# Kernel optimization log

Measured on AMD Instinct MI355X. Metric: run time of the kernel, lower is better.

The kernel has to match this reference:

```python
import jax, jax.numpy as jnp
import numpy as np

N_NODES = 50000
IN_F, HID_F, OUT_F = 256, 128, 40
N_EDGES = 800000


def _uniform(key, shape, scale):
    return jax.random.uniform(key, shape, dtype=jnp.float32, minval=-scale, maxval=scale)


def setup_inputs() -> dict:
    key = jax.random.key(0)
    ks = jax.random.split(key, 20)
    x = jax.random.normal(ks[0], (N_NODES, IN_F), dtype=jnp.float32)
    edge_index = jax.random.randint(ks[1], (2, N_EDGES), 0, N_NODES, dtype=jnp.int64)
    s0, sa0 = 1.0 / np.sqrt(HID_F), 1.0  # std_att = 1/sqrt(1)
    s1, sa1 = 1.0 / np.sqrt(OUT_F), 1.0
    sv = 1.0 / np.sqrt(3.0)
    return {
        "x": x, "edge_index": edge_index,
        "Wl0": _uniform(ks[2], (IN_F, HID_F), s0),
        "Wh0": _uniform(ks[3], (IN_F, HID_F), s0),
        "Wm0": _uniform(ks[4], (IN_F, HID_F), s0),
        "al0": _uniform(ks[5], (HID_F, 1), sa0),
        "ah0": _uniform(ks[6], (HID_F, 1), sa0),
        "am0": _uniform(ks[7], (HID_F, 1), sa0),
        "att0": _uniform(ks[8], (3, 3), sv),
        "Wl1": _uniform(ks[9], (HID_F, OUT_F), s1),
        "Wh1": _uniform(ks[10], (HID_F, OUT_F), s1),
        "Wm1": _uniform(ks[11], (HID_F, OUT_F), s1),
        "al1": _uniform(ks[12], (OUT_F, 1), sa1),
        "ah1": _uniform(ks[13], (OUT_F, 1), sa1),
        "am1": _uniform(ks[14], (OUT_F, 1), sa1),
        "att1": _uniform(ks[15], (3, 3), sv),
    }


def _acm_layer(x, row, col, d_inv, Wl, Wh, Wm, al, ah, am, att):
    n = x.shape[0]
    hl, hh, hm = x @ Wl, x @ Wh, x @ Wm
    # adj_low @ M  with adj_low = D^{-1}(I + A): gather sources, scatter-add to rows
    def low(M):
        return d_inv[:, None] * (M + jax.ops.segment_sum(M[col], row, num_segments=n))
    out_low = jax.nn.relu(low(hl))
    out_high = jax.nn.relu(hh - low(hh))  # adj_high = I - adj_low
    out_mlp = jax.nn.relu(hm)
    T = 3.0
    sig = jax.nn.sigmoid(jnp.concatenate([out_low @ al, out_high @ ah, out_mlp @ am], axis=1))  # [n,3]
    a = jax.nn.softmax((sig @ att) / T, axis=1)
    return 3.0 * (a[:, 0:1] * out_low + a[:, 1:2] * out_high + a[:, 2:3] * out_mlp)


def reference(x, edge_index, Wl0, Wh0, Wm0, al0, ah0, am0, att0,
              Wl1, Wh1, Wm1, al1, ah1, am1, att1):
    n = x.shape[0]
    row, col = edge_index[0], edge_index[1]
    deg = jax.ops.segment_sum(jnp.ones_like(row, dtype=jnp.float32), row, num_segments=n)
    rowsum = 1.0 + deg  # rowsum of I + A (duplicates counted, as in scipy)
    d_inv = jnp.where(rowsum > 0, 1.0 / rowsum, 0.0)
    h = _acm_layer(x, row, col, d_inv, Wl0, Wh0, Wm0, al0, ah0, am0, att0)
    out = _acm_layer(h, row, col, d_inv, Wl1, Wh1, Wm1, al1, ah1, am1, att1)
    return out
```

## Files before the change

kernel.cpp:

```cpp
#include <hip/hip_runtime.h>
#include <math.h>

#define N_NODES 50000
#define N_EDGES 800000
#define IN_F    256
#define HID_F   128
#define OUT_F   40
#define W0N     (3*HID_F)
#define W1N     (3*OUT_F)
#define NB      ((N_NODES + 255) / 256)

#define XB   6250
#define P0B  ((IN_F * W0N) / 256)
#define P1B  ((HID_F * W1N) / 256)
#define CB0  (XB + P0B + P1B)
#define CNTB ((N_EDGES + 255) / 256)
#define PREPB (CB0 + CNTB)

typedef __attribute__((ext_vector_type(8))) unsigned short ushort8;
typedef __attribute__((ext_vector_type(4))) unsigned short ushort4v;
typedef __attribute__((ext_vector_type(8))) __bf16 bf16x8;
typedef __attribute__((ext_vector_type(4))) float f32x4;
typedef __attribute__((ext_vector_type(2))) float f32x2;

static __device__ __forceinline__ float sigmoidf_(float x) {
    return 1.0f / (1.0f + expf(-x));
}

static __device__ __forceinline__ unsigned short f2bf(float f) {
    unsigned u = __float_as_uint(f);
    u += 0x7FFFu + ((u >> 16) & 1u);
    return (unsigned short)(u >> 16);
}

static __device__ __forceinline__ float bflo(unsigned u) { return __uint_as_float(u << 16); }
static __device__ __forceinline__ float bfhi(unsigned u) { return __uint_as_float(u & 0xffff0000u); }


__global__ __launch_bounds__(256) void k_prep(
        const float* __restrict__ x, unsigned short* __restrict__ xb,
        const float* __restrict__ Wl0, const float* __restrict__ Wh0,
        const float* __restrict__ Wm0, unsigned short* __restrict__ W0t,
        const float* __restrict__ Wl1, const float* __restrict__ Wh1,
        const float* __restrict__ Wm1, unsigned short* __restrict__ W1t,
        const int* __restrict__ ei, int* __restrict__ deg,
        unsigned short* __restrict__ rank, unsigned* __restrict__ rc) {
    int b = blockIdx.x, t = threadIdx.x;
    if (b < XB) {
        size_t idx = (size_t)b * 2048 + t * 8;
        float4 f0 = *(const float4*)(x + idx);
        float4 f1 = *(const float4*)(x + idx + 4);
        ushort8 u;
        u[0]=f2bf(f0.x); u[1]=f2bf(f0.y); u[2]=f2bf(f0.z); u[3]=f2bf(f0.w);
        u[4]=f2bf(f1.x); u[5]=f2bf(f1.y); u[6]=f2bf(f1.z); u[7]=f2bf(f1.w);
        *(ushort8*)(xb + idx) = u;
    } else if (b < XB + P0B) {
        int i = (b - XB) * 256 + t;
        int n = i / IN_F, k = i % IN_F;
        float v;
        if (n < HID_F)            v = Wl0[k * HID_F + n];
        else if (n < 2 * HID_F)   v = Wh0[k * HID_F + (n - HID_F)];
        else                      v = Wm0[k * HID_F + (n - 2 * HID_F)];
        W0t[i] = f2bf(v);
    } else if (b < CB0) {
        int i = (b - XB - P0B) * 256 + t;
        int n = i / HID_F, kp = i % HID_F;
        int k = ((kp >> 6) << 6) + ((kp & 3) << 4) + ((kp >> 2) & 15);
        float v;
        if (n < OUT_F)            v = Wl1[k * OUT_F + n];
        else if (n < 2 * OUT_F)   v = Wh1[k * OUT_F + (n - OUT_F)];
        else                      v = Wm1[k * OUT_F + (n - 2 * OUT_F)];
        W1t[i] = f2bf(v);
    } else {
        int e = (b - CB0) * 256 + t;
        if (e < N_EDGES) {
            int r = ei[e];
            int c = ei[N_EDGES + e];
            int old = atomicAdd(&deg[r], 1);
            rank[e] = (unsigned short)old;
            rc[e] = ((unsigned)r << 16) | (unsigned)c;
        }
    }
}


__global__ void k_scan1(const int* __restrict__ deg, int* __restrict__ rowPtr,
                        int* __restrict__ blkTot, float* __restrict__ dinv) {
    __shared__ int s[256];
    int t = threadIdx.x;
    int gid = blockIdx.x * 256 + t;
    int v = (gid < N_NODES) ? deg[gid] : 0;
    if (gid < N_NODES) dinv[gid] = 1.0f / (1.0f + (float)v);
    s[t] = v; __syncthreads();
    for (int d = 1; d < 256; d <<= 1) {
        int x = (t >= d) ? s[t - d] : 0;
        __syncthreads();
        s[t] += x;
        __syncthreads();
    }
    if (gid < N_NODES) rowPtr[gid] = s[t];
    if (t == 255) blkTot[blockIdx.x] = s[255];
}

__global__ void k_scan2(int* __restrict__ blk) {
    __shared__ int s[256];
    int t = threadIdx.x;
    int v = (t < NB) ? blk[t] : 0;
    s[t] = v; __syncthreads();
    for (int d = 1; d < 256; d <<= 1) {
        int x = (t >= d) ? s[t - d] : 0;
        __syncthreads();
        s[t] += x;
        __syncthreads();
    }
    if (t < NB) blk[t] = s[t] - v;
}

__global__ void k_scan3(const int* __restrict__ deg, const int* __restrict__ blkOff,
                        int* __restrict__ rowPtr) {
    int t = threadIdx.x;
    int gid = blockIdx.x * 256 + t;
    if (gid < N_NODES) rowPtr[gid] += blkOff[blockIdx.x] - deg[gid];
    if (gid == 0) rowPtr[N_NODES] = N_EDGES;
}


#define BKP 40

template<int EPI>
__global__ __launch_bounds__(256) void k_gemm_fill(
        const unsigned short* __restrict__ A, const unsigned short* __restrict__ Bt,
        unsigned short* __restrict__ C0, int ld0,
        unsigned short* __restrict__ C1, int ld1, int nsplit,
        unsigned short* __restrict__ Hs, unsigned char* __restrict__ Hq,
        unsigned short* __restrict__ HmP,
        int M, int N, int K, int nxt,
        const unsigned* __restrict__ rc, const unsigned short* __restrict__ rank,
        const int* __restrict__ rowPtr, unsigned short* __restrict__ colIdx) {
    __shared__ unsigned short As[128 * BKP];
    __shared__ unsigned short Bs[128 * BKP];
    int tid  = threadIdx.x;

    if ((int)blockIdx.x >= nxt) {
        int fid = (blockIdx.x - nxt) * gridDim.y + blockIdx.y;
        int e = fid * 256 + tid;
        if (e < N_EDGES) {
            unsigned x = rc[e];
            int r = (int)(x >> 16);
            int pos = rowPtr[r] + (int)rank[e];
            colIdx[pos] = (unsigned short)(x & 0xffffu);
        }
        return;
    }

    int lane = tid & 63, wid = tid >> 6;
    int wr = wid >> 1, wc = wid & 1;
    int bm = blockIdx.y * 128, bn = blockIdx.x * 128;

    int srow = tid >> 1;
    int scol = (tid & 1) * 16;

    int garow = min(bm + srow, M - 1);
    int gbrow = min(bn + srow, N - 1);

    f32x4 acc[4][4];
#pragma unroll
    for (int m = 0; m < 4; ++m)
#pragma unroll
        for (int n = 0; n < 4; ++n)
            acc[m][n] = (f32x4)(0.0f);

    int kg = (lane >> 4) * 8;
    int rA = wr * 64 + (lane & 15);
    int rB = wc * 64 + (lane & 15);

    for (int k0 = 0; k0 < K; k0 += 32) {
        {
            const unsigned short* src = A + (size_t)garow * K + k0 + scol;
            *(ushort8*)&As[srow * BKP + scol]     = *(const ushort8*)(src);
            *(ushort8*)&As[srow * BKP + scol + 8] = *(const ushort8*)(src + 8);
        }
        {
            const unsigned short* src = Bt + (size_t)gbrow * K + k0 + scol;
            *(ushort8*)&Bs[srow * BKP + scol]     = *(const ushort8*)(src);
            *(ushort8*)&Bs[srow * BKP + scol + 8] = *(const ushort8*)(src + 8);
        }
        __syncthreads();

        bf16x8 a[4], b[4];
#pragma unroll
        for (int m = 0; m < 4; ++m)
            a[m] = __builtin_bit_cast(bf16x8, *(const ushort8*)&As[(rA + m * 16) * BKP + kg]);
#pragma unroll
        for (int n = 0; n < 4; ++n)
            b[n] = __builtin_bit_cast(bf16x8, *(const ushort8*)&Bs[(rB + n * 16) * BKP + kg]);
#pragma unroll
        for (int m = 0; m < 4; ++m)
#pragma unroll
            for (int n = 0; n < 4; ++n)
                acc[m][n] = __builtin_amdgcn_mfma_f32_16x16x32_bf16(a[m], b[n], acc[m][n], 0, 0, 0);
        __syncthreads();
    }

    int col  = lane & 15;
    int rsub = (lane >> 4) * 4;

    if (EPI == 0) {
#pragma unroll
        for (int m = 0; m < 4; ++m) {
            int gm0 = bm + wr * 64 + m * 16 + rsub;
#pragma unroll
            for (int n = 0; n < 4; ++n) {
                int gn = bn + wc * 64 + n * 16 + col;
                if (gn >= N) continue;
#pragma unroll
                for (int j = 0; j < 4; ++j) {
                    int gm = gm0 + j;
                    if (gm >= M) continue;
                    unsigned short b = f2bf(acc[m][n][j]);
                    if (gn < nsplit) C0[(size_t)gm * ld0 + gn] = b;
                    else             C1[(size_t)gm * ld1 + (gn - nsplit)] = b;
                }
            }
        }
    } else {
#pragma unroll
        for (int m = 0; m < 4; ++m) {
            int gm0 = bm + wr * 64 + m * 16 + rsub;
#pragma unroll
            for (int j = 0; j < 4; ++j) {
                int gm = gm0 + j;
                if (gm >= M) continue;
                float v0 = acc[m][0][j], v1 = acc[m][1][j];
                float v2 = acc[m][2][j], v3 = acc[m][3][j];
                ushort4v o;
                o[0] = f2bf(v0); o[1] = f2bf(v1); o[2] = f2bf(v2); o[3] = f2bf(v3);
                if (bn < 256) {
                    int pos = bn + wc * 64 + col * 4;
                    *(ushort4v*)&Hs[(size_t)gm * 256 + pos] = o;
                    int pk = 0;
                    pk = __builtin_amdgcn_cvt_pk_fp8_f32(v0, v1, pk, false);
                    pk = __builtin_amdgcn_cvt_pk_fp8_f32(v2, v3, pk, true);
                    *(unsigned*)&Hq[(size_t)gm * 256 + pos] = (unsigned)pk;
                } else {
                    int pos = wc * 64 + col * 4;
                    *(ushort4v*)&HmP[(size_t)gm * 128 + pos] = o;
                }
            }
        }
    }
}


__global__ __launch_bounds__(256) void k_layer0(
        const unsigned short* __restrict__ Hs, const unsigned char* __restrict__ Hq,
        const unsigned short* __restrict__ HmP,
        const int* __restrict__ rowPtr, const unsigned short* __restrict__ colIdx,
        const float* __restrict__ dinv,
        const float* __restrict__ al, const float* __restrict__ ah,
        const float* __restrict__ am, const float* __restrict__ att,
        unsigned short* __restrict__ hout) {
    int lane = threadIdx.x & 63;
    int i = blockIdx.x * 4 + (threadIdx.x >> 6);

    int p0 = rowPtr[i], p1 = rowPtr[i + 1];
    float a0 = 0.f, a1 = 0.f, a2 = 0.f, a3 = 0.f;
    int off4 = lane * 4;
    int p = p0;
    for (; p + 7 < p1; p += 8) {
        int j[8];
#pragma unroll
        for (int q = 0; q < 8; ++q) j[q] = (int)colIdx[p + q];
        unsigned w[8];
#pragma unroll
        for (int q = 0; q < 8; ++q) w[q] = *(const unsigned*)(Hq + (size_t)j[q] * 256 + off4);
#pragma unroll
        for (int q = 0; q < 8; ++q) {
            f32x2 d0 = __builtin_amdgcn_cvt_pk_f32_fp8((int)w[q], false);
            f32x2 d1 = __builtin_amdgcn_cvt_pk_f32_fp8((int)w[q], true);
            a0 += d0.x; a1 += d0.y; a2 += d1.x; a3 += d1.y;
        }
    }
    for (; p < p1; ++p) {
        int j = (int)colIdx[p];
        unsigned w = *(const unsigned*)(Hq + (size_t)j * 256 + off4);
        f32x2 d0 = __builtin_amdgcn_cvt_pk_f32_fp8((int)w, false);
        f32x2 d1 = __builtin_amdgcn_cvt_pk_f32_fp8((int)w, true);
        a0 += d0.x; a1 += d0.y; a2 += d1.x; a3 += d1.y;
    }

    uint2 sv = *(const uint2*)(Hs + (size_t)i * 256 + off4);
    float s0 = bflo(sv.x), s1 = bfhi(sv.x), s2 = bflo(sv.y), s3 = bfhi(sv.y);
    float di = dinv[i];
    float l0 = di * (s0 + a0), l1 = di * (s1 + a1);
    float l2 = di * (s2 + a2), l3 = di * (s3 + a3);

    float ol0 = fmaxf(l0, 0.f), ol1 = fmaxf(l1, 0.f);
    float ol2 = fmaxf(l2, 0.f), ol3 = fmaxf(l3, 0.f);
    float oh0 = fmaxf(s0 - l0, 0.f), oh1 = fmaxf(s1 - l1, 0.f);
    float oh2 = fmaxf(s2 - l2, 0.f), oh3 = fmaxf(s3 - l3, 0.f);

    int c0 = ((lane >> 4) << 6) + (lane & 15);

    float om0 = 0.f, om1 = 0.f, om2 = 0.f, om3 = 0.f;
    float prA, prM = 0.f;
    if (lane < 32) {
        uint2 hv = *(const uint2*)(HmP + (size_t)i * 128 + off4);
        om0 = fmaxf(bflo(hv.x), 0.f); om1 = fmaxf(bfhi(hv.x), 0.f);
        om2 = fmaxf(bflo(hv.y), 0.f); om3 = fmaxf(bfhi(hv.y), 0.f);
        prA = ol0 * al[c0] + ol1 * al[c0 + 16] + ol2 * al[c0 + 32] + ol3 * al[c0 + 48];
        prM = om0 * am[c0] + om1 * am[c0 + 16] + om2 * am[c0 + 32] + om3 * am[c0 + 48];
    } else {
        int ch = c0 - 128;
        prA = oh0 * ah[ch] + oh1 * ah[ch + 16] + oh2 * ah[ch + 32] + oh3 * ah[ch + 48];
    }

#pragma unroll
    for (int d = 1; d < 32; d <<= 1) prA += __shfl_xor(prA, d);
#pragma unroll
    for (int d = 1; d < 32; d <<= 1) prM += __shfl_xor(prM, d);
    float g0 = __shfl(prA, 0);
    float g1 = __shfl(prA, 32);
    float g2 = __shfl(prM, 0);

    float sg0 = sigmoidf_(g0), sg1 = sigmoidf_(g1), sg2 = sigmoidf_(g2);
    const float inv3 = (1.0f / 3.0f);
    float e0 = (sg0 * att[0] + sg1 * att[3] + sg2 * att[6]) * inv3;
    float e1 = (sg0 * att[1] + sg1 * att[4] + sg2 * att[7]) * inv3;
    float e2 = (sg0 * att[2] + sg1 * att[5] + sg2 * att[8]) * inv3;
    float mx = fmaxf(e0, fmaxf(e1, e2));
    float x0 = expf(e0 - mx), x1 = expf(e1 - mx), x2 = expf(e2 - mx);
    float inv = 1.0f / (x0 + x1 + x2);
    float c0f = 3.0f * inv * x0, c1f = 3.0f * inv * x1, c2f = 3.0f * inv * x2;

    int src = lane | 32;
    float th0 = __shfl(oh0, src), th1 = __shfl(oh1, src);
    float th2 = __shfl(oh2, src), th3 = __shfl(oh3, src);

    if (lane < 32) {
        ushort4v o;
        o[0] = f2bf(c0f * ol0 + c1f * th0 + c2f * om0);
        o[1] = f2bf(c0f * ol1 + c1f * th1 + c2f * om1);
        o[2] = f2bf(c0f * ol2 + c1f * th2 + c2f * om2);
        o[3] = f2bf(c0f * ol3 + c1f * th3 + c2f * om3);
        *(ushort4v*)&hout[(size_t)i * 128 + off4] = o;
    }
}


__global__ __launch_bounds__(256) void k_layer1(
        const unsigned short* __restrict__ H1g, const unsigned short* __restrict__ H1m,
        const int* __restrict__ rowPtr, const unsigned short* __restrict__ colIdx,
        const float* __restrict__ dinv,
        const float* __restrict__ al, const float* __restrict__ ah,
        const float* __restrict__ am, const float* __restrict__ att,
        float* __restrict__ out) {
    int lane = threadIdx.x & 63;
    int i = blockIdx.x * 4 + (threadIdx.x >> 6);

    int p0 = rowPtr[i], p1 = rowPtr[i + 1];
    float a0 = 0.f, a1 = 0.f;
    int off = lane * 2;
    bool active = lane < 40;
    int p = p0;
    if (active) {
        for (; p + 7 < p1; p += 8) {
            int j[8];
#pragma unroll
            for (int q = 0; q < 8; ++q) j[q] = (int)colIdx[p + q];
            unsigned v[8];
#pragma unroll
            for (int q = 0; q < 8; ++q) v[q] = *(const unsigned*)(H1g + (size_t)j[q] * 80 + off);
#pragma unroll
            for (int q = 0; q < 8; ++q) { a0 += bflo(v[q]); a1 += bfhi(v[q]); }
        }
        for (; p < p1; ++p) {
            int j = (int)colIdx[p];
            unsigned v = *(const unsigned*)(H1g + (size_t)j * 80 + off);
            a0 += bflo(v); a1 += bfhi(v);
        }
    }

    float s0 = 0.f, s1 = 0.f;
    if (active) {
        unsigned sv = *(const unsigned*)(H1g + (size_t)i * 80 + off);
        s0 = bflo(sv); s1 = bfhi(sv);
    }
    float di = dinv[i];
    float l0 = di * (s0 + a0), l1 = di * (s1 + a1);

    float ol0 = fmaxf(l0, 0.f), ol1 = fmaxf(l1, 0.f);
    float oh0 = fmaxf(s0 - l0, 0.f), oh1 = fmaxf(s1 - l1, 0.f);

    float om0 = 0.f, om1 = 0.f;
    float r0 = 0.f, r1 = 0.f, r2 = 0.f;
    if (lane < 20) {
        unsigned hv = *(const unsigned*)(H1m + (size_t)i * 40 + off);
        om0 = fmaxf(bflo(hv), 0.f); om1 = fmaxf(bfhi(hv), 0.f);
        float2 alv = *(const float2*)(al + off);
        float2 amv = *(const float2*)(am + off);
        r0 = ol0 * alv.x + ol1 * alv.y;
        r2 = om0 * amv.x + om1 * amv.y;
    } else if (lane < 40) {
        float2 ahv = *(const float2*)(ah + (off - 40));
        r1 = oh0 * ahv.x + oh1 * ahv.y;
    }

#pragma unroll
    for (int d = 1; d < 64; d <<= 1) r0 += __shfl_xor(r0, d);
#pragma unroll
    for (int d = 1; d < 64; d <<= 1) r1 += __shfl_xor(r1, d);
#pragma unroll
    for (int d = 1; d < 64; d <<= 1) r2 += __shfl_xor(r2, d);

    float sg0 = sigmoidf_(r0), sg1 = sigmoidf_(r1), sg2 = sigmoidf_(r2);
    const float inv3 = (1.0f / 3.0f);
    float e0 = (sg0 * att[0] + sg1 * att[3] + sg2 * att[6]) * inv3;
    float e1 = (sg0 * att[1] + sg1 * att[4] + sg2 * att[7]) * inv3;
    float e2 = (sg0 * att[2] + sg1 * att[5] + sg2 * att[8]) * inv3;
    float mx = fmaxf(e0, fmaxf(e1, e2));
    float x0 = expf(e0 - mx), x1 = expf(e1 - mx), x2 = expf(e2 - mx);
    float inv = 1.0f / (x0 + x1 + x2);
    float c0 = 3.0f * inv * x0, c1 = 3.0f * inv * x1, c2 = 3.0f * inv * x2;

    int src = (lane + 20) & 63;
    float th0 = __shfl(oh0, src), th1 = __shfl(oh1, src);

    if (lane < 20) {
        float2 o;
        o.x = c0 * ol0 + c1 * th0 + c2 * om0;
        o.y = c0 * ol1 + c1 * th1 + c2 * om1;
        *(float2*)&out[(size_t)i * 40 + off] = o;
    }
}


extern "C" void kernel_launch(void* const* d_in, const int* in_sizes, int n_in,
                              void* d_out, int out_size, void* d_ws, size_t ws_size,
                              hipStream_t stream) {
    const float* x    = (const float*)d_in[0];
    const int*   ei   = (const int*)d_in[1];
    const float* Wl0  = (const float*)d_in[2];
    const float* Wh0  = (const float*)d_in[3];
    const float* Wm0  = (const float*)d_in[4];
    const float* al0  = (const float*)d_in[5];
    const float* ah0  = (const float*)d_in[6];
    const float* am0  = (const float*)d_in[7];
    const float* att0 = (const float*)d_in[8];
    const float* Wl1  = (const float*)d_in[9];
    const float* Wh1  = (const float*)d_in[10];
    const float* Wm1  = (const float*)d_in[11];
    const float* al1  = (const float*)d_in[12];
    const float* ah1  = (const float*)d_in[13];
    const float* am1  = (const float*)d_in[14];
    const float* att1 = (const float*)d_in[15];
    float* out = (float*)d_out;

    char* ws = (char*)d_ws;
    size_t off = 0;
    auto alloc = [&](size_t bytes) -> char* {
        char* p = ws + off;
        off += (bytes + 255) & ~(size_t)255;
        return p;
    };
    int*   deg    = (int*)  alloc((size_t)N_NODES * 4);
    int*   rowPtr = (int*)  alloc((size_t)(N_NODES + 1) * 4);
    int*   blkTot = (int*)  alloc(256 * 4);
    unsigned short* rank   = (unsigned short*)alloc((size_t)N_EDGES * 2);
    unsigned*       rc     = (unsigned*)      alloc((size_t)N_EDGES * 4);
    unsigned short* colIdx = (unsigned short*)alloc((size_t)N_EDGES * 2);
    float* dinv   = (float*)alloc((size_t)N_NODES * 4);
    unsigned short* W0t  = (unsigned short*)alloc((size_t)W0N * IN_F * 2);
    unsigned short* W1t  = (unsigned short*)alloc((size_t)W1N * HID_F * 2);
    unsigned short* xb   = (unsigned short*)alloc((size_t)N_NODES * IN_F * 2);
    unsigned short* Hs   = (unsigned short*)alloc((size_t)N_NODES * 256 * 2);
    unsigned char*  Hq   = (unsigned char*) alloc((size_t)N_NODES * 256);
    unsigned short* HmP  = (unsigned short*)alloc((size_t)N_NODES * 128 * 2);
    unsigned short* H1g  = (unsigned short*)alloc((size_t)N_NODES * 80 * 2);
    unsigned short* H1m  = (unsigned short*)alloc((size_t)N_NODES * 40 * 2);
    unsigned short* hbuf = (unsigned short*)alloc((size_t)N_NODES * HID_F * 2);

    hipMemsetAsync(deg, 0, (size_t)N_NODES * 4, stream);
    k_prep<<<PREPB, 256, 0, stream>>>(x, xb, Wl0, Wh0, Wm0, W0t,
                                      Wl1, Wh1, Wm1, W1t, ei, deg, rank, rc);
    k_scan1<<<NB, 256, 0, stream>>>(deg, rowPtr, blkTot, dinv);
    k_scan2<<<1, 256, 0, stream>>>(blkTot);
    k_scan3<<<NB, 256, 0, stream>>>(deg, blkTot, rowPtr);
    {
        dim3 grid(3 + 8, (N_NODES + 127) / 128);
        k_gemm_fill<1><<<grid, 256, 0, stream>>>(xb, W0t,
                                                 nullptr, 0, nullptr, 0, 0,
                                                 Hs, Hq, HmP,
                                                 N_NODES, W0N, IN_F, 3,
                                                 rc, rank, rowPtr, colIdx);
    }
    k_layer0<<<N_NODES / 4, 256, 0, stream>>>(Hs, Hq, HmP, rowPtr, colIdx, dinv,
                                              al0, ah0, am0, att0, hbuf);
    {
        dim3 grid(1, (N_NODES + 127) / 128);
        k_gemm_fill<0><<<grid, 256, 0, stream>>>(hbuf, W1t,
                                                 H1g, 80, H1m, 40, 80,
                                                 nullptr, nullptr, nullptr,
                                                 N_NODES, W1N, HID_F, 1,
                                                 nullptr, nullptr, nullptr, nullptr);
    }
    k_layer1<<<N_NODES / 4, 256, 0, stream>>>(H1g, H1m, rowPtr, colIdx, dinv,
                                              al1, ah1, am1, att1, out);
}
```

Baseline: 213.5 us.

## Build CSR via per-segment shared-memory histograms instead of global atomics

```diff
diff --git a/kernel.cpp b/kernel.cpp
--- a/kernel.cpp
+++ b/kernel.cpp
@@ -10,12 +10,15 @@
 #define W1N     (3*OUT_F)
 #define NB      ((N_NODES + 255) / 256)
 
-#define XB   6250
+#define SEG     128
+#define EPB     (N_EDGES / SEG)
+#define NWORD   (N_NODES / 2)
+#define WB      ((NWORD + 255) / 256)
+
+#define XB   ((N_NODES * IN_F) / (256 * 16))
 #define P0B  ((IN_F * W0N) / 256)
 #define P1B  ((HID_F * W1N) / 256)
-#define CB0  (XB + P0B + P1B)
-#define CNTB ((N_EDGES + 255) / 256)
-#define PREPB (CB0 + CNTB)
+#define PREPB (XB + P0B + P1B)
 
 typedef __attribute__((ext_vector_type(8))) unsigned short ushort8;
 typedef __attribute__((ext_vector_type(4))) unsigned short ushort4v;
@@ -37,23 +40,106 @@
 static __device__ __forceinline__ float bfhi(unsigned u) { return __uint_as_float(u & 0xffff0000u); }
 
 
+__global__ __launch_bounds__(256) void k_hist(
+        const int* __restrict__ ei, unsigned* __restrict__ segHist,
+        unsigned short* __restrict__ rank, unsigned* __restrict__ rc) {
+    __shared__ unsigned hist[NWORD];
+    int t = threadIdx.x, seg = blockIdx.x;
+    for (int i = t; i < NWORD; i += 256) hist[i] = 0;
+    __syncthreads();
+    int base = seg * EPB;
+    for (int k = t; k < EPB; k += 256) {
+        int e = base + k;
+        int r = ei[e];
+        int c = ei[N_EDGES + e];
+        unsigned old = atomicAdd(&hist[r >> 1], (r & 1) ? 0x10000u : 1u);
+        unsigned lr = (r & 1) ? (old >> 16) : (old & 0xffffu);
+        rank[e] = (unsigned short)lr;
+        rc[e] = ((unsigned)r << 16) | (unsigned)c;
+    }
+    __syncthreads();
+    unsigned* dst = segHist + (size_t)seg * NWORD;
+    for (int i = t; i < NWORD; i += 256) dst[i] = hist[i];
+}
+
+
+__global__ __launch_bounds__(256) void k_scanseg(
+        unsigned* __restrict__ segHist, int* __restrict__ rowPtr,
+        float* __restrict__ dinv, int* __restrict__ blkTot) {
+    __shared__ int s[256];
+    int t = threadIdx.x;
+    int w = blockIdx.x * 256 + t;
+    int cum0 = 0, cum1 = 0;
+    if (w < NWORD) {
+        for (int sg = 0; sg < SEG; ++sg) {
+            size_t idx = (size_t)sg * NWORD + w;
+            unsigned h = segHist[idx];
+            segHist[idx] = ((unsigned)cum1 << 16) | (unsigned)cum0;
+            cum0 += (int)(h & 0xffffu);
+            cum1 += (int)(h >> 16);
+        }
+    }
+    int deg0 = cum0, deg1 = cum1;
+    int pair = deg0 + deg1;
+    s[t] = pair; __syncthreads();
+    for (int d = 1; d < 256; d <<= 1) {
+        int x = (t >= d) ? s[t - d] : 0;
+        __syncthreads();
+        s[t] += x;
+        __syncthreads();
+    }
+    int basep = s[t] - pair;
+    if (w < NWORD) {
+        rowPtr[2 * w]     = basep;
+        rowPtr[2 * w + 1] = basep + deg0;
+        dinv[2 * w]     = 1.0f / (1.0f + (float)deg0);
+        dinv[2 * w + 1] = 1.0f / (1.0f + (float)deg1);
+    }
+    if (t == 255) blkTot[blockIdx.x] = s[255];
+}
+
+__global__ void k_scan2(int* __restrict__ blk) {
+    __shared__ int s[256];
+    int t = threadIdx.x;
+    int v = (t < WB) ? blk[t] : 0;
+    s[t] = v; __syncthreads();
+    for (int d = 1; d < 256; d <<= 1) {
+        int x = (t >= d) ? s[t - d] : 0;
+        __syncthreads();
+        s[t] += x;
+        __syncthreads();
+    }
+    if (t < WB) blk[t] = s[t] - v;
+}
+
+__global__ void k_scan3(const int* __restrict__ blkOff, int* __restrict__ rowPtr) {
+    int t = threadIdx.x;
+    int gid = blockIdx.x * 256 + t;
+    if (gid < N_NODES) rowPtr[gid] += blkOff[gid >> 9];
+    if (gid == 0) rowPtr[N_NODES] = N_EDGES;
+}
+
+
 __global__ __launch_bounds__(256) void k_prep(
         const float* __restrict__ x, unsigned short* __restrict__ xb,
         const float* __restrict__ Wl0, const float* __restrict__ Wh0,
         const float* __restrict__ Wm0, unsigned short* __restrict__ W0t,
         const float* __restrict__ Wl1, const float* __restrict__ Wh1,
-        const float* __restrict__ Wm1, unsigned short* __restrict__ W1t,
-        const int* __restrict__ ei, int* __restrict__ deg,
-        unsigned short* __restrict__ rank, unsigned* __restrict__ rc) {
+        const float* __restrict__ Wm1, unsigned short* __restrict__ W1t) {
     int b = blockIdx.x, t = threadIdx.x;
     if (b < XB) {
-        size_t idx = (size_t)b * 2048 + t * 8;
+        size_t idx = (size_t)b * 4096 + t * 16;
         float4 f0 = *(const float4*)(x + idx);
         float4 f1 = *(const float4*)(x + idx + 4);
-        ushort8 u;
-        u[0]=f2bf(f0.x); u[1]=f2bf(f0.y); u[2]=f2bf(f0.z); u[3]=f2bf(f0.w);
-        u[4]=f2bf(f1.x); u[5]=f2bf(f1.y); u[6]=f2bf(f1.z); u[7]=f2bf(f1.w);
-        *(ushort8*)(xb + idx) = u;
+        float4 f2 = *(const float4*)(x + idx + 8);
+        float4 f3 = *(const float4*)(x + idx + 12);
+        ushort8 u0, u1;
+        u0[0]=f2bf(f0.x); u0[1]=f2bf(f0.y); u0[2]=f2bf(f0.z); u0[3]=f2bf(f0.w);
+        u0[4]=f2bf(f1.x); u0[5]=f2bf(f1.y); u0[6]=f2bf(f1.z); u0[7]=f2bf(f1.w);
+        u1[0]=f2bf(f2.x); u1[1]=f2bf(f2.y); u1[2]=f2bf(f2.z); u1[3]=f2bf(f2.w);
+        u1[4]=f2bf(f3.x); u1[5]=f2bf(f3.y); u1[6]=f2bf(f3.z); u1[7]=f2bf(f3.w);
+        *(ushort8*)(xb + idx)     = u0;
+        *(ushort8*)(xb + idx + 8) = u1;
     } else if (b < XB + P0B) {
         int i = (b - XB) * 256 + t;
         int n = i / IN_F, k = i % IN_F;
@@ -62,7 +148,7 @@
         else if (n < 2 * HID_F)   v = Wh0[k * HID_F + (n - HID_F)];
         else                      v = Wm0[k * HID_F + (n - 2 * HID_F)];
         W0t[i] = f2bf(v);
-    } else if (b < CB0) {
+    } else {
         int i = (b - XB - P0B) * 256 + t;
         int n = i / HID_F, kp = i % HID_F;
         int k = ((kp >> 6) << 6) + ((kp & 3) << 4) + ((kp >> 2) & 15);
@@ -71,57 +157,7 @@
         else if (n < 2 * OUT_F)   v = Wh1[k * OUT_F + (n - OUT_F)];
         else                      v = Wm1[k * OUT_F + (n - 2 * OUT_F)];
         W1t[i] = f2bf(v);
-    } else {
-        int e = (b - CB0) * 256 + t;
-        if (e < N_EDGES) {
-            int r = ei[e];
-            int c = ei[N_EDGES + e];
-            int old = atomicAdd(&deg[r], 1);
-            rank[e] = (unsigned short)old;
-            rc[e] = ((unsigned)r << 16) | (unsigned)c;
-        }
-    }
-}
-
-
-__global__ void k_scan1(const int* __restrict__ deg, int* __restrict__ rowPtr,
-                        int* __restrict__ blkTot, float* __restrict__ dinv) {
-    __shared__ int s[256];
-    int t = threadIdx.x;
-    int gid = blockIdx.x * 256 + t;
-    int v = (gid < N_NODES) ? deg[gid] : 0;
-    if (gid < N_NODES) dinv[gid] = 1.0f / (1.0f + (float)v);
-    s[t] = v; __syncthreads();
-    for (int d = 1; d < 256; d <<= 1) {
-        int x = (t >= d) ? s[t - d] : 0;
-        __syncthreads();
-        s[t] += x;
-        __syncthreads();
-    }
-    if (gid < N_NODES) rowPtr[gid] = s[t];
-    if (t == 255) blkTot[blockIdx.x] = s[255];
-}
-
-__global__ void k_scan2(int* __restrict__ blk) {
-    __shared__ int s[256];
-    int t = threadIdx.x;
-    int v = (t < NB) ? blk[t] : 0;
-    s[t] = v; __syncthreads();
-    for (int d = 1; d < 256; d <<= 1) {
-        int x = (t >= d) ? s[t - d] : 0;
-        __syncthreads();
-        s[t] += x;
-        __syncthreads();
-    }
-    if (t < NB) blk[t] = s[t] - v;
-}
-
-__global__ void k_scan3(const int* __restrict__ deg, const int* __restrict__ blkOff,
-                        int* __restrict__ rowPtr) {
-    int t = threadIdx.x;
-    int gid = blockIdx.x * 256 + t;
-    if (gid < N_NODES) rowPtr[gid] += blkOff[blockIdx.x] - deg[gid];
-    if (gid == 0) rowPtr[N_NODES] = N_EDGES;
+    }
 }
 
 
@@ -136,7 +172,8 @@
         unsigned short* __restrict__ HmP,
         int M, int N, int K, int nxt,
         const unsigned* __restrict__ rc, const unsigned short* __restrict__ rank,
-        const int* __restrict__ rowPtr, unsigned short* __restrict__ colIdx) {
+        const int* __restrict__ rowPtr, const unsigned short* __restrict__ segOff,
+        unsigned short* __restrict__ colIdx) {
     __shared__ unsigned short As[128 * BKP];
     __shared__ unsigned short Bs[128 * BKP];
     int tid  = threadIdx.x;
@@ -147,7 +184,8 @@
         if (e < N_EDGES) {
             unsigned x = rc[e];
             int r = (int)(x >> 16);
-            int pos = rowPtr[r] + (int)rank[e];
+            int seg = e / EPB;
+            int pos = rowPtr[r] + (int)segOff[(size_t)seg * N_NODES + r] + (int)rank[e];
             colIdx[pos] = (unsigned short)(x & 0xffffu);
         }
         return;
@@ -463,9 +501,9 @@
         off += (bytes + 255) & ~(size_t)255;
         return p;
     };
-    int*   deg    = (int*)  alloc((size_t)N_NODES * 4);
-    int*   rowPtr = (int*)  alloc((size_t)(N_NODES + 1) * 4);
-    int*   blkTot = (int*)  alloc(256 * 4);
+    int*      rowPtr  = (int*)     alloc((size_t)(N_NODES + 1) * 4);
+    int*      blkTot  = (int*)     alloc(256 * 4);
+    unsigned* segHist = (unsigned*)alloc((size_t)SEG * NWORD * 4);
     unsigned short* rank   = (unsigned short*)alloc((size_t)N_EDGES * 2);
     unsigned*       rc     = (unsigned*)      alloc((size_t)N_EDGES * 4);
     unsigned short* colIdx = (unsigned short*)alloc((size_t)N_EDGES * 2);
@@ -480,19 +518,20 @@
     unsigned short* H1m  = (unsigned short*)alloc((size_t)N_NODES * 40 * 2);
     unsigned short* hbuf = (unsigned short*)alloc((size_t)N_NODES * HID_F * 2);
 
-    hipMemsetAsync(deg, 0, (size_t)N_NODES * 4, stream);
+    k_hist<<<SEG, 256, 0, stream>>>(ei, segHist, rank, rc);
     k_prep<<<PREPB, 256, 0, stream>>>(x, xb, Wl0, Wh0, Wm0, W0t,
-                                      Wl1, Wh1, Wm1, W1t, ei, deg, rank, rc);
-    k_scan1<<<NB, 256, 0, stream>>>(deg, rowPtr, blkTot, dinv);
+                                      Wl1, Wh1, Wm1, W1t);
+    k_scanseg<<<WB, 256, 0, stream>>>(segHist, rowPtr, dinv, blkTot);
     k_scan2<<<1, 256, 0, stream>>>(blkTot);
-    k_scan3<<<NB, 256, 0, stream>>>(deg, blkTot, rowPtr);
+    k_scan3<<<NB, 256, 0, stream>>>(blkTot, rowPtr);
     {
         dim3 grid(3 + 8, (N_NODES + 127) / 128);
         k_gemm_fill<1><<<grid, 256, 0, stream>>>(xb, W0t,
                                                  nullptr, 0, nullptr, 0, 0,
                                                  Hs, Hq, HmP,
                                                  N_NODES, W0N, IN_F, 3,
-                                                 rc, rank, rowPtr, colIdx);
+                                                 rc, rank, rowPtr,
+                                                 (const unsigned short*)segHist, colIdx);
     }
     k_layer0<<<N_NODES / 4, 256, 0, stream>>>(Hs, Hq, HmP, rowPtr, colIdx, dinv,
                                               al0, ah0, am0, att0, hbuf);
@@ -502,7 +541,7 @@
                                                  H1g, 80, H1m, 40, 80,
                                                  nullptr, nullptr, nullptr,
                                                  N_NODES, W1N, HID_F, 1,
-                                                 nullptr, nullptr, nullptr, nullptr);
+                                                 nullptr, nullptr, nullptr, nullptr, nullptr);
     }
     k_layer1<<<N_NODES / 4, 256, 0, stream>>>(H1g, H1m, rowPtr, colIdx, dinv,
                                               al1, ah1, am1, att1, out);
```

After: 201.8 us. -5.5%, faster.
